# Optimization experiments

Hardware: AMD Instinct MI355X
Metric: run time of the kernel (lower is better)

## Reference

```python
import jax, jax.numpy as jnp
import numpy as np

L, B, D, H, P = 4096, 4, 1024, 16, 256
HD = D // H
EPS = 1e-5


def _layer_norm(x, g, b):
    m = jnp.mean(x, axis=-1, keepdims=True)
    v = jnp.mean(jnp.square(x - m), axis=-1, keepdims=True)
    return (x - m) / jnp.sqrt(v + EPS) * g + b


def setup_inputs() -> dict:
    key = jax.random.key(0)
    ks = jax.random.split(key, 8)
    w = lambda k, shape: jax.random.normal(k, shape, jnp.float32) * 0.02
    return {
        "query": jax.random.normal(ks[0], (L, B, D), jnp.float32),
        "q_w": w(ks[1], (D, D)), "q_b": jnp.zeros((D,), jnp.float32),
        "k_w": w(ks[2], (D, D)), "k_b": jnp.zeros((D,), jnp.float32),
        "v_w": w(ks[3], (D, D)), "v_b": jnp.zeros((D,), jnp.float32),
        "e_weight": w(ks[4], (1, H, P, HD)),
        "e_out_w": w(ks[5], (D, D)), "e_out_b": jnp.zeros((D,), jnp.float32),
        "ln_g": jnp.ones((D,), jnp.float32), "ln_b": jnp.zeros((D,), jnp.float32),
        "out_w": w(ks[6], (D, D)), "out_b": jnp.zeros((D,), jnp.float32),
    }


def reference(query, q_w, q_b, k_w, k_b, v_w, v_b, e_weight,
              e_out_w, e_out_b, ln_g, ln_b, out_w, out_b):
    scaling = HD ** -0.5
    # ---- _compute_kv (kv_same=True, no padding mask) ----
    # kv: (L,B,D) -> (B,H,HD,L)
    kvh = query.reshape(L, B, H, HD).transpose(1, 2, 3, 0)
    # pkv = relu(E @ (kv * scaling)) : (B,H,P,L)
    pkv = jax.nn.relu(jnp.einsum('hpd,bhdl->bhpl', e_weight[0], kvh * scaling))
    # kv = pkv @ kv^T : (B,H,P,HD)
    kv = jnp.einsum('bhpl,bhdl->bhpd', pkv, kvh)
    # -> (P,B,D), e_out linear, residual add of e_weight, layer norm
    kv = kv.transpose(2, 0, 1, 3).reshape(P, B, D)
    kv = kv @ e_out_w.T + e_out_b
    kv = kv.reshape(P, B, H, HD) + e_weight.transpose(2, 0, 1, 3)  # broadcast (P,1,H,HD)
    kv = _layer_norm(kv.reshape(P, B, D), ln_g, ln_b)  # (P,B,D)

    # ---- standard MHA against the compressed kv ----
    q = (query @ q_w.T + q_b) * scaling            # (L,B,D)
    k = kv @ k_w.T + k_b                           # (P,B,D)
    v = kv @ v_w.T + v_b                           # (P,B,D)
    qh = q.reshape(L, B, H, HD)
    kh = k.reshape(P, B, H, HD)
    vh = v.reshape(P, B, H, HD)
    logits = jnp.einsum('lbhd,pbhd->bhlp', qh, kh)
    probs = jax.nn.softmax(logits, axis=-1)
    attn = jnp.einsum('bhlp,pbhd->lbhd', probs, vh).reshape(L, B, D)
    return attn @ out_w.T + out_b
```

## Files before the change

kernel.cpp:

```cpp
#include <hip/hip_runtime.h>
#include <hip/hip_bf16.h>
#include <cstdint>
#include <cstddef>

#define LL 4096
#define BB 4
#define DD 1024
#define HH 16
#define PP 256
#define HDD 64
#define LC 16
#define LCHUNK 256

constexpr float kScaling = 0.125f;
constexpr float kEps = 1e-5f;

typedef __attribute__((ext_vector_type(8))) short bf16x8;
typedef __attribute__((ext_vector_type(4))) short short4v;
typedef __attribute__((ext_vector_type(4))) float f32x4;

#define MFMA16(a, b, c) __builtin_amdgcn_mfma_f32_16x16x32_bf16((a), (b), (c), 0, 0, 0)

__device__ __forceinline__ unsigned short f2bf(float f) {
  unsigned int u = __builtin_bit_cast(unsigned int, f);
  u += 0x7FFFu + ((u >> 16) & 1u);
  return (unsigned short)(u >> 16);
}

__device__ __forceinline__ void gll16(const void* g, void* l) {
  __builtin_amdgcn_global_load_lds(
      (const __attribute__((address_space(1))) unsigned int*)g,
      (__attribute__((address_space(3))) unsigned int*)l, 16, 0, 0);
}

__global__ __launch_bounds__(256) void k_cvt(const float* __restrict__ src,
                                             unsigned short* __restrict__ dst,
                                             int n8) {
  int i = blockIdx.x * 256 + threadIdx.x;
  if (i >= n8) return;
  const float4* s = (const float4*)(src + (size_t)i * 8);
  float4 a = s[0], b = s[1];
  bf16x8 o;
  o[0] = f2bf(a.x); o[1] = f2bf(a.y); o[2] = f2bf(a.z); o[3] = f2bf(a.w);
  o[4] = f2bf(b.x); o[5] = f2bf(b.y); o[6] = f2bf(b.z); o[7] = f2bf(b.w);
  *(bf16x8*)(dst + (size_t)i * 8) = o;
}

__global__ __launch_bounds__(256) void k_compress_mfma(
    const unsigned short* __restrict__ qbf, const unsigned short* __restrict__ ewbf,
    float* __restrict__ parts) {
  const int bh = blockIdx.x, lc = blockIdx.y;
  const int b = bh >> 4, h = bh & 15;
  const int tid = threadIdx.x, wv = tid >> 6, lane = tid & 63;
  const int fr = lane & 15, fg = lane >> 4;

  __shared__ __align__(16) char Xl[8192];
  __shared__ __align__(16) char Xtl[8192];
  __shared__ __align__(16) char Pl[32768];

  bf16x8 ef[4][2];
#pragma unroll
  for (int pt = 0; pt < 4; ++pt)
#pragma unroll
    for (int kc = 0; kc < 2; ++kc)
      ef[pt][kc] = *(const bf16x8*)(ewbf +
          (size_t)((h * PP + wv * 64 + pt * 16 + fr) * HDD) + kc * 32 + fg * 8);

  f32x4 acc[4][4];
#pragma unroll
  for (int i = 0; i < 4; ++i)
#pragma unroll
    for (int j = 0; j < 4; ++j) acc[i][j] = (f32x4){0.f, 0.f, 0.f, 0.f};

  const int l0 = lc * LCHUNK;
  for (int t = 0; t < 4; ++t) {
    __syncthreads();
#pragma unroll
    for (int j = 0; j < 2; ++j) {
      int u = tid + j * 256;
      int l = u >> 3, c8 = u & 7;
      bf16x8 val = *(const bf16x8*)(qbf +
          ((size_t)(l0 + t * 64 + l) * BB + b) * DD + h * HDD + c8 * 8);
      *(bf16x8*)(Xl + l * 128 + ((c8 ^ (l & 7)) << 4)) = val;
#pragma unroll
      for (int i = 0; i < 8; ++i) {
        int dd = c8 * 8 + i;
        *(short*)(Xtl + dd * 128 + ((((l >> 3) ^ (dd & 7) ^ (dd >> 3)) & 7) << 4) +
                  ((l & 7) << 1)) = val[i];
      }
    }
    __syncthreads();
#pragma unroll
    for (int lt = 0; lt < 4; ++lt) {
      int rl = lt * 16 + fr;
      bf16x8 xa0 = *(const bf16x8*)(Xl + rl * 128 + (((0 + fg) ^ (rl & 7)) << 4));
      bf16x8 xa1 = *(const bf16x8*)(Xl + rl * 128 + (((4 + fg) ^ (rl & 7)) << 4));
#pragma unroll
      for (int pt = 0; pt < 4; ++pt) {
        f32x4 s = (f32x4){0.f, 0.f, 0.f, 0.f};
        s = MFMA16(xa0, ef[pt][0], s);
        s = MFMA16(xa1, ef[pt][1], s);
        short4v pk;
#pragma unroll
        for (int r = 0; r < 4; ++r)
          pk[r] = (short)f2bf(fmaxf(s[r] * kScaling, 0.f));
        int p = wv * 64 + pt * 16 + fr;
        int lbase = lt * 16 + fg * 4;
        int slot = lbase >> 3;
        *(short4v*)(Pl + p * 128 + ((slot ^ (p & 7)) << 4) + ((lbase & 7) << 1)) = pk;
      }
    }
    asm volatile("s_waitcnt lgkmcnt(0)" ::: "memory");
    __builtin_amdgcn_sched_barrier(0);
#pragma unroll
    for (int kc = 0; kc < 2; ++kc) {
      bf16x8 pa[4], xb[4];
#pragma unroll
      for (int pt = 0; pt < 4; ++pt) {
        int p = wv * 64 + pt * 16 + fr;
        pa[pt] = *(const bf16x8*)(Pl + p * 128 + (((kc * 4 + fg) ^ (p & 7)) << 4));
      }
#pragma unroll
      for (int dt = 0; dt < 4; ++dt) {
        int dd = dt * 16 + fr;
        xb[dt] = *(const bf16x8*)(Xtl + dd * 128 +
                  ((((kc * 4 + fg) ^ (dd & 7) ^ (dd >> 3)) & 7) << 4));
      }
#pragma unroll
      for (int pt = 0; pt < 4; ++pt)
#pragma unroll
        for (int dt = 0; dt < 4; ++dt)
          acc[pt][dt] = MFMA16(pa[pt], xb[dt], acc[pt][dt]);
    }
  }
  float* op = parts + (size_t)(lc * 64 + bh) * PP * HDD;
#pragma unroll
  for (int pt = 0; pt < 4; ++pt)
#pragma unroll
    for (int dt = 0; dt < 4; ++dt)
#pragma unroll
      for (int r = 0; r < 4; ++r) {
        int p = wv * 64 + pt * 16 + fg * 4 + r;
        int dd = dt * 16 + fr;
        op[(size_t)p * HDD + dd] = acc[pt][dt][r];
      }
}

__global__ __launch_bounds__(256) void k_reduce(const float* __restrict__ parts,
                                                unsigned short* __restrict__ kv_raw_bf) {
  int i = blockIdx.x * 256 + threadIdx.x;
  float s = 0.f;
#pragma unroll
  for (int lcc = 0; lcc < LC; ++lcc) s += parts[(size_t)lcc * (64 * PP * HDD) + i];
  int d = i & 63, p = (i >> 6) & 255, bh = i >> 14;
  int b = bh >> 4, h = bh & 15;
  kv_raw_bf[(size_t)(p * BB + b) * DD + h * HDD + d] = f2bf(s);
}

template <int MODE, typename OUTT>
__device__ __forceinline__ void gemm_body(
    const unsigned short* __restrict__ A, const unsigned short* __restrict__ W,
    const float* __restrict__ bias, const float* __restrict__ ew,
    OUTT* __restrict__ C, int m0, int n0, char* Al, char* Bl) {
  const int tid = threadIdx.x;
  const int wv = tid >> 6, lane = tid & 63;
  const int fr = lane & 15, fg = lane >> 4;
  const int wr = wv >> 1, wc = wv & 1;

  f32x4 acc[4][4];
#pragma unroll
  for (int i = 0; i < 4; ++i)
#pragma unroll
    for (int j = 0; j < 4; ++j) acc[i][j] = (f32x4){0.f, 0.f, 0.f, 0.f};

  for (int k0 = 0; k0 < DD; k0 += 64) {
    __syncthreads();
#pragma unroll
    for (int j = 0; j < 4; ++j) {
      int u = tid + j * 256;
      int row = u >> 3, slot = u & 7;
      size_t gcol = (size_t)(k0 + 8 * (slot ^ (row & 7)));
      gll16(A + (size_t)(m0 + row) * DD + gcol, Al + u * 16);
      gll16(W + (size_t)(n0 + row) * DD + gcol, Bl + u * 16);
    }
    __syncthreads();
#pragma unroll
    for (int kc = 0; kc < 2; ++kc) {
      bf16x8 af[4], bfr[4];
#pragma unroll
      for (int mt = 0; mt < 4; ++mt) {
        int r = wr * 64 + mt * 16 + fr;
        af[mt] = *(const bf16x8*)(Al + r * 128 + (((kc * 4 + fg) ^ (r & 7)) << 4));
      }
#pragma unroll
      for (int nt = 0; nt < 4; ++nt) {
        int r = wc * 64 + nt * 16 + fr;
        bfr[nt] = *(const bf16x8*)(Bl + r * 128 + (((kc * 4 + fg) ^ (r & 7)) << 4));
      }
#pragma unroll
      for (int mt = 0; mt < 4; ++mt)
#pragma unroll
        for (int nt = 0; nt < 4; ++nt)
          acc[mt][nt] = MFMA16(af[mt], bfr[nt], acc[mt][nt]);
    }
  }

  float bs[4];
#pragma unroll
  for (int nt = 0; nt < 4; ++nt) bs[nt] = bias[n0 + wc * 64 + nt * 16 + fr];
#pragma unroll
  for (int mt = 0; mt < 4; ++mt)
#pragma unroll
    for (int nt = 0; nt < 4; ++nt) {
      int n = n0 + wc * 64 + nt * 16 + fr;
#pragma unroll
      for (int r = 0; r < 4; ++r) {
        int m = m0 + wr * 64 + mt * 16 + fg * 4 + r;
        float v = acc[mt][nt][r] + bs[nt];
        if (MODE == 1) v *= kScaling;
        if (MODE == 2) {
          int p = m >> 2, hh = n >> 6, d2 = n & 63;
          v += ew[(size_t)((hh << 8) + p) * HDD + d2];
        }
        if constexpr (sizeof(OUTT) == 2)
          C[(size_t)m * DD + n] = (OUTT)f2bf(v);
        else
          C[(size_t)m * DD + n] = v;
      }
    }
}

template <int MODE, typename OUTT>
__global__ __launch_bounds__(256) void k_gemm_mfma(
    const unsigned short* __restrict__ A, const unsigned short* __restrict__ W,
    const float* __restrict__ bias, const float* __restrict__ ew,
    OUTT* __restrict__ C) {
  __shared__ __align__(16) char Al[16384];
  __shared__ __align__(16) char Bl[16384];
  gemm_body<MODE, OUTT>(A, W, bias, ew, C, blockIdx.x * 128, blockIdx.y * 128, Al, Bl);
}

__global__ __launch_bounds__(256) void k_gemm_kv(
    const unsigned short* __restrict__ A,
    const unsigned short* __restrict__ Wk, const unsigned short* __restrict__ Wv,
    const float* __restrict__ kb, const float* __restrict__ vb,
    unsigned short* __restrict__ Ck, unsigned short* __restrict__ Cv) {
  __shared__ __align__(16) char Al[16384];
  __shared__ __align__(16) char Bl[16384];
  if (blockIdx.z == 0)
    gemm_body<0, unsigned short>(A, Wk, kb, nullptr, Ck,
                                 blockIdx.x * 128, blockIdx.y * 128, Al, Bl);
  else
    gemm_body<0, unsigned short>(A, Wv, vb, nullptr, Cv,
                                 blockIdx.x * 128, blockIdx.y * 128, Al, Bl);
}

__global__ __launch_bounds__(256) void k_ln(const float* __restrict__ x,
                                            const float* __restrict__ g,
                                            const float* __restrict__ bb,
                                            unsigned short* __restrict__ y) {
  const int r = blockIdx.x;
  const int tid = threadIdx.x;
  const float* xr = x + (size_t)r * DD;
  float4 v = *(const float4*)(xr + tid * 4);
  float s1 = v.x + v.y + v.z + v.w;
  float s2 = v.x * v.x + v.y * v.y + v.z * v.z + v.w * v.w;
#pragma unroll
  for (int off = 32; off > 0; off >>= 1) {
    s1 += __shfl_down(s1, off);
    s2 += __shfl_down(s2, off);
  }
  __shared__ float w1[4], w2[4];
  if ((tid & 63) == 0) { w1[tid >> 6] = s1; w2[tid >> 6] = s2; }
  __syncthreads();
  float S1 = w1[0] + w1[1] + w1[2] + w1[3];
  float S2 = w2[0] + w2[1] + w2[2] + w2[3];
  float mean = S1 * (1.f / DD);
  float var = S2 * (1.f / DD) - mean * mean;
  float rstd = rsqrtf(var + kEps);
  float4 gv = *(const float4*)(g + tid * 4);
  float4 bv = *(const float4*)(bb + tid * 4);
  short4v o;
  o[0] = (short)f2bf((v.x - mean) * rstd * gv.x + bv.x);
  o[1] = (short)f2bf((v.y - mean) * rstd * gv.y + bv.y);
  o[2] = (short)f2bf((v.z - mean) * rstd * gv.z + bv.z);
  o[3] = (short)f2bf((v.w - mean) * rstd * gv.w + bv.w);
  *(short4v*)(y + (size_t)r * DD + tid * 4) = o;
}

__global__ __launch_bounds__(512, 2) void k_attn_mfma(
    const unsigned short* __restrict__ qbf, const unsigned short* __restrict__ kbf,
    const unsigned short* __restrict__ vbf, unsigned short* __restrict__ attn) {
  const int bh = blockIdx.y;
  const int b = bh >> 4, h = bh & 15;
  const int tid = threadIdx.x, wv = tid >> 6, lane = tid & 63;
  const int fr = lane & 15, fg = lane >> 4;
  const int bl0 = blockIdx.x * 128;

  __shared__ __align__(16) char Kl[16384];
  __shared__ __align__(16) char Vt[16384];
  __shared__ __align__(16) char Pl[32768];

  const size_t qrow = ((size_t)(bl0 + wv * 16 + fr) * BB + b) * DD + h * HDD;
  bf16x8 qf0 = *(const bf16x8*)(qbf + qrow + fg * 8);
  bf16x8 qf1 = *(const bf16x8*)(qbf + qrow + 32 + fg * 8);

  f32x4 o[4];
#pragma unroll
  for (int dt = 0; dt < 4; ++dt) o[dt] = (f32x4){0.f, 0.f, 0.f, 0.f};
  float psum = 0.f;
  char* Pw = Pl + wv * 4096;

  for (int ph = 0; ph < 2; ++ph) {
    __syncthreads();
#pragma unroll
    for (int j = 0; j < 2; ++j) {
      int u = tid + j * 512;
      int p = u >> 3, slot = u & 7;
      gll16(kbf + ((size_t)((ph * 128 + p) * BB + b)) * DD + h * HDD +
                8 * (slot ^ (p & 7)),
            Kl + u * 16);
    }
#pragma unroll
    for (int j = 0; j < 2; ++j) {
      int u = tid + j * 512;
      int p = u >> 3, c8 = u & 7;
      bf16x8 val = *(const bf16x8*)(vbf +
          ((size_t)((ph * 128 + p) * BB + b)) * DD + h * HDD + c8 * 8);
      int pc = p >> 6, pl = p & 63;
#pragma unroll
      for (int i = 0; i < 8; ++i) {
        int dd = c8 * 8 + i;
        *(short*)(Vt + pc * 8192 + dd * 128 +
                  ((((pl >> 3) ^ (dd & 7) ^ (dd >> 3)) & 7) << 4) +
                  ((pl & 7) << 1)) = val[i];
      }
    }
    __syncthreads();

    f32x4 s[8];
    __builtin_amdgcn_s_setprio(1);
#pragma unroll
    for (int pt = 0; pt < 8; ++pt) {
      int pr = pt * 16 + fr;
      bf16x8 a0 = *(const bf16x8*)(Kl + pr * 128 + ((fg ^ (pr & 7)) << 4));
      bf16x8 a1 = *(const bf16x8*)(Kl + pr * 128 + (((4 + fg) ^ (pr & 7)) << 4));
      f32x4 acc = (f32x4){0.f, 0.f, 0.f, 0.f};
      acc = MFMA16(a0, qf0, acc);
      acc = MFMA16(a1, qf1, acc);
      s[pt] = acc;
    }
    __builtin_amdgcn_s_setprio(0);

#pragma unroll
    for (int pt = 0; pt < 8; ++pt) {
      float e0 = __expf(s[pt][0]), e1 = __expf(s[pt][1]);
      float e2 = __expf(s[pt][2]), e3 = __expf(s[pt][3]);
      psum += (e0 + e1) + (e2 + e3);
      short4v pk;
      pk[0] = (short)f2bf(e0); pk[1] = (short)f2bf(e1);
      pk[2] = (short)f2bf(e2); pk[3] = (short)f2bf(e3);
      int pbyte = (pt * 16 + fg * 4) * 2;
      int slot = pbyte >> 4, rem = pbyte & 15;
      *(short4v*)(Pw + fr * 256 + ((slot ^ (fr & 7)) << 4) + rem) = pk;
    }
    asm volatile("s_waitcnt lgkmcnt(0)" ::: "memory");
    __builtin_amdgcn_sched_barrier(0);

    __builtin_amdgcn_s_setprio(1);
#pragma unroll
    for (int kc = 0; kc < 4; ++kc) {
      int slot = kc * 4 + fg;
      bf16x8 pa = *(const bf16x8*)(Pw + fr * 256 + ((slot ^ (fr & 7)) << 4));
      int sl2 = (kc & 1) * 4 + fg;
#pragma unroll
      for (int dt = 0; dt < 4; ++dt) {
        int dd = dt * 16 + fr;
        bf16x8 vb = *(const bf16x8*)(Vt + (kc >> 1) * 8192 + dd * 128 +
                     (((sl2 ^ (dd & 7) ^ (dd >> 3)) & 7) << 4));
        o[dt] = MFMA16(pa, vb, o[dt]);
      }
    }
    __builtin_amdgcn_s_setprio(0);
  }

  psum += __shfl_xor(psum, 16);
  psum += __shfl_xor(psum, 32);

#pragma unroll
  for (int r = 0; r < 4; ++r) {
    int lloc = fg * 4 + r;
    float inv = 1.f / __shfl(psum, lloc);
    unsigned short* op = attn +
        ((size_t)(bl0 + wv * 16 + lloc) * BB + b) * DD + h * HDD;
#pragma unroll
    for (int dt = 0; dt < 4; ++dt)
      op[dt * 16 + fr] = f2bf(o[dt][r] * inv);
  }
}

extern "C" void kernel_launch(void* const* d_in, const int* in_sizes, int n_in,
                              void* d_out, int out_size, void* d_ws, size_t ws_size,
                              hipStream_t stream) {
  const float* query   = (const float*)d_in[0];
  const float* q_w     = (const float*)d_in[1];
  const float* q_b     = (const float*)d_in[2];
  const float* k_w     = (const float*)d_in[3];
  const float* k_b     = (const float*)d_in[4];
  const float* v_w     = (const float*)d_in[5];
  const float* v_b     = (const float*)d_in[6];
  const float* e_weight= (const float*)d_in[7];
  const float* e_out_w = (const float*)d_in[8];
  const float* e_out_b = (const float*)d_in[9];
  const float* ln_g    = (const float*)d_in[10];
  const float* ln_b    = (const float*)d_in[11];
  const float* out_w   = (const float*)d_in[12];
  const float* out_b   = (const float*)d_in[13];
  float* out = (float*)d_out;

  char* w = (char*)d_ws;
  float* parts            = (float*)w;
  unsigned short* q_bf    = (unsigned short*)w;
  unsigned short* attn_bf = (unsigned short*)(w + (32u << 20));
  unsigned short* query_bf= (unsigned short*)(w + (64u << 20));
  unsigned short* kv_raw  = (unsigned short*)(w + (96u << 20));
  float* kv_eo            = (float*)(w + (98u << 20));
  unsigned short* kv_ln   = (unsigned short*)(w + (102u << 20));
  unsigned short* k_buf   = (unsigned short*)(w + (104u << 20));
  unsigned short* v_buf   = (unsigned short*)(w + (106u << 20));
  unsigned short* wq  = (unsigned short*)(w + (108u << 20));
  unsigned short* wk  = (unsigned short*)(w + (110u << 20));
  unsigned short* wv_ = (unsigned short*)(w + (112u << 20));
  unsigned short* weo = (unsigned short*)(w + (114u << 20));
  unsigned short* wo  = (unsigned short*)(w + (116u << 20));
  unsigned short* ewb = (unsigned short*)(w + (118u << 20));

  k_cvt<<<8192, 256, 0, stream>>>(query, query_bf, 2097152);
  k_cvt<<<512, 256, 0, stream>>>(q_w, wq, 131072);
  k_cvt<<<512, 256, 0, stream>>>(k_w, wk, 131072);
  k_cvt<<<512, 256, 0, stream>>>(v_w, wv_, 131072);
  k_cvt<<<512, 256, 0, stream>>>(e_out_w, weo, 131072);
  k_cvt<<<512, 256, 0, stream>>>(out_w, wo, 131072);
  k_cvt<<<128, 256, 0, stream>>>(e_weight, ewb, 32768);

  k_compress_mfma<<<dim3(64, LC), 256, 0, stream>>>(query_bf, ewb, parts);
  k_reduce<<<4096, 256, 0, stream>>>(parts, kv_raw);
  k_gemm_mfma<2, float><<<dim3(8, 8), 256, 0, stream>>>(kv_raw, weo, e_out_b, e_weight, kv_eo);
  k_ln<<<PP * BB, 256, 0, stream>>>(kv_eo, ln_g, ln_b, kv_ln);
  k_gemm_mfma<1, unsigned short><<<dim3(128, 8), 256, 0, stream>>>(query_bf, wq, q_b, nullptr, q_bf);
  k_gemm_kv<<<dim3(8, 8, 2), 256, 0, stream>>>(kv_ln, wk, wv_, k_b, v_b, k_buf, v_buf);
  k_attn_mfma<<<dim3(32, 64), 512, 0, stream>>>(q_bf, k_buf, v_buf, attn_bf);
  k_gemm_mfma<0, float><<<dim3(128, 8), 256, 0, stream>>>(attn_bf, wo, out_b, nullptr, out);
}
```

Before: 247.9 us.

## Use 256x256 tiled GEMM with triple-buffered async loads for Q and output projections

Adds a 512-thread GEMM kernel that computes a 256x256 output tile per block. It uses a 128 KB LDS double/triple-staged pipeline with direct global-to-LDS loads, XOR-swizzled layout, and interleaved MFMA phases with barriers and priority hints. The large Q projection and output projection GEMMs now use it instead of the 128x128 kernel. This aims to raise arithmetic intensity and overlap memory with compute. In exchange, the 256-block grid may underfill the CUs, the LDS footprint is large, and the register pressure is high.

```diff
diff --git a/kernel.cpp b/kernel.cpp
--- a/kernel.cpp
+++ b/kernel.cpp
@@ -253,6 +253,152 @@
   else
     gemm_body<0, unsigned short>(A, Wv, vb, nullptr, Cv,
                                  blockIdx.x * 128, blockIdx.y * 128, Al, Bl);
+}
+
+template <int MODE, typename OUTT>
+__global__ __launch_bounds__(512, 2) void k_gemm256(
+    const unsigned short* __restrict__ A, const unsigned short* __restrict__ W,
+    const float* __restrict__ bias, OUTT* __restrict__ C) {
+  __shared__ __align__(16) char lds[131072];
+  const int tid = threadIdx.x;
+  const int wv = tid >> 6, lane = tid & 63;
+  const int fr = lane & 15, fg = lane >> 4;
+  const int wm = wv >> 2, wn = wv & 3;
+  const int m0 = blockIdx.x * 256, n0 = blockIdx.y * 256;
+  const int srow = tid >> 2, sslot = tid & 3;
+
+  auto stageHalf = [&](const unsigned short* __restrict__ G, int g0, int colbase,
+                       int dstBase) {
+#pragma unroll
+    for (int j = 0; j < 2; ++j) {
+      int row = srow + j * 128;
+      int gs = sslot ^ ((row >> 1) & 3);
+      gll16(G + (size_t)(g0 + row) * DD + colbase + gs * 8,
+            lds + dstBase + (tid + j * 512) * 16);
+    }
+  };
+  auto rdA = [&](int mf, int kc, int cb) -> bf16x8 {
+    int r = wm * 128 + mf * 16 + fr;
+    return *(const bf16x8*)(lds + cb + kc * 16384 + r * 64 +
+                            ((fg ^ ((r >> 1) & 3)) << 4));
+  };
+  auto rdB = [&](int nf, int kc, int cb) -> bf16x8 {
+    int r = wn * 64 + nf * 16 + fr;
+    return *(const bf16x8*)(lds + cb + 32768 + kc * 16384 + r * 64 +
+                            ((fg ^ ((r >> 1) & 3)) << 4));
+  };
+
+  f32x4 acc[8][4];
+#pragma unroll
+  for (int i = 0; i < 8; ++i)
+#pragma unroll
+    for (int j = 0; j < 4; ++j) acc[i][j] = (f32x4){0.f, 0.f, 0.f, 0.f};
+  bf16x8 a[4], b[4];
+
+  stageHalf(A, m0, 0, 0);
+  stageHalf(W, n0, 0, 32768);
+  stageHalf(A, m0, 32, 16384);
+  stageHalf(W, n0, 32, 32768 + 16384);
+  stageHalf(A, m0, 64, 65536);
+  stageHalf(W, n0, 64, 65536 + 32768);
+  asm volatile("s_waitcnt vmcnt(4)" ::: "memory");
+  __builtin_amdgcn_s_barrier();
+
+  const int NT = DD / 64;
+  for (int t = 0; t < NT; ++t) {
+    const int cb = (t & 1) << 16;
+    const int nb = cb ^ 65536;
+    const int k1 = (t + 1) * 64, k2 = (t + 2) * 64;
+
+#pragma unroll
+    for (int i = 0; i < 4; ++i) a[i] = rdA(i, 0, cb);
+#pragma unroll
+    for (int i = 0; i < 4; ++i) b[i] = rdB(i, 0, cb);
+    if (t + 1 < NT) stageHalf(A, m0, k1 + 32, nb + 16384);
+    __builtin_amdgcn_s_barrier();
+    asm volatile("s_waitcnt lgkmcnt(0)" ::: "memory");
+    __builtin_amdgcn_sched_barrier(0);
+    __builtin_amdgcn_s_setprio(1);
+#pragma unroll
+    for (int mf = 0; mf < 4; ++mf)
+#pragma unroll
+      for (int nf = 0; nf < 4; ++nf)
+        acc[mf][nf] = MFMA16(a[mf], b[nf], acc[mf][nf]);
+    __builtin_amdgcn_s_setprio(0);
+    __builtin_amdgcn_s_barrier();
+
+#pragma unroll
+    for (int i = 0; i < 4; ++i) a[i] = rdA(4 + i, 0, cb);
+    if (t + 1 < NT) stageHalf(W, n0, k1 + 32, nb + 32768 + 16384);
+    __builtin_amdgcn_s_barrier();
+    asm volatile("s_waitcnt lgkmcnt(0)" ::: "memory");
+    __builtin_amdgcn_sched_barrier(0);
+    __builtin_amdgcn_s_setprio(1);
+#pragma unroll
+    for (int mf = 0; mf < 4; ++mf)
+#pragma unroll
+      for (int nf = 0; nf < 4; ++nf)
+        acc[4 + mf][nf] = MFMA16(a[mf], b[nf], acc[4 + mf][nf]);
+    __builtin_amdgcn_s_setprio(0);
+    __builtin_amdgcn_s_barrier();
+
+#pragma unroll
+    for (int i = 0; i < 4; ++i) a[i] = rdA(i, 1, cb);
+#pragma unroll
+    for (int i = 0; i < 4; ++i) b[i] = rdB(i, 1, cb);
+    if (t + 2 < NT) stageHalf(A, m0, k2, cb);
+    __builtin_amdgcn_s_barrier();
+    asm volatile("s_waitcnt lgkmcnt(0)" ::: "memory");
+    __builtin_amdgcn_sched_barrier(0);
+    __builtin_amdgcn_s_setprio(1);
+#pragma unroll
+    for (int mf = 0; mf < 4; ++mf)
+#pragma unroll
+      for (int nf = 0; nf < 4; ++nf)
+        acc[mf][nf] = MFMA16(a[mf], b[nf], acc[mf][nf]);
+    __builtin_amdgcn_s_setprio(0);
+    __builtin_amdgcn_s_barrier();
+
+#pragma unroll
+    for (int i = 0; i < 4; ++i) a[i] = rdA(4 + i, 1, cb);
+    if (t + 2 < NT) stageHalf(W, n0, k2, cb + 32768);
+    __builtin_amdgcn_s_barrier();
+    asm volatile("s_waitcnt lgkmcnt(0)" ::: "memory");
+    __builtin_amdgcn_sched_barrier(0);
+    __builtin_amdgcn_s_setprio(1);
+#pragma unroll
+    for (int mf = 0; mf < 4; ++mf)
+#pragma unroll
+      for (int nf = 0; nf < 4; ++nf)
+        acc[4 + mf][nf] = MFMA16(a[mf], b[nf], acc[4 + mf][nf]);
+    __builtin_amdgcn_s_setprio(0);
+    if (t + 2 < NT) {
+      asm volatile("s_waitcnt vmcnt(4)" ::: "memory");
+    } else if (t + 1 < NT) {
+      asm volatile("s_waitcnt vmcnt(0)" ::: "memory");
+    }
+    __builtin_amdgcn_s_barrier();
+  }
+
+  float bs[4];
+#pragma unroll
+  for (int nf = 0; nf < 4; ++nf) bs[nf] = bias[n0 + wn * 64 + nf * 16 + fr];
+#pragma unroll
+  for (int mf = 0; mf < 8; ++mf)
+#pragma unroll
+    for (int nf = 0; nf < 4; ++nf) {
+      int n = n0 + wn * 64 + nf * 16 + fr;
+#pragma unroll
+      for (int r = 0; r < 4; ++r) {
+        int m = m0 + wm * 128 + mf * 16 + fg * 4 + r;
+        float v = acc[mf][nf][r] + bs[nf];
+        if (MODE == 1) v *= kScaling;
+        if constexpr (sizeof(OUTT) == 2)
+          C[(size_t)m * DD + n] = (OUTT)f2bf(v);
+        else
+          C[(size_t)m * DD + n] = v;
+      }
+    }
 }
 
 __global__ __launch_bounds__(256) void k_ln(const float* __restrict__ x,
@@ -447,8 +593,8 @@
   k_reduce<<<4096, 256, 0, stream>>>(parts, kv_raw);
   k_gemm_mfma<2, float><<<dim3(8, 8), 256, 0, stream>>>(kv_raw, weo, e_out_b, e_weight, kv_eo);
   k_ln<<<PP * BB, 256, 0, stream>>>(kv_eo, ln_g, ln_b, kv_ln);
-  k_gemm_mfma<1, unsigned short><<<dim3(128, 8), 256, 0, stream>>>(query_bf, wq, q_b, nullptr, q_bf);
+  k_gemm256<1, unsigned short><<<dim3(64, 4), 512, 0, stream>>>(query_bf, wq, q_b, q_bf);
   k_gemm_kv<<<dim3(8, 8, 2), 256, 0, stream>>>(kv_ln, wk, wv_, k_b, v_b, k_buf, v_buf);
   k_attn_mfma<<<dim3(32, 64), 512, 0, stream>>>(q_bf, k_buf, v_buf, attn_bf);
-  k_gemm_mfma<0, float><<<dim3(128, 8), 256, 0, stream>>>(attn_bf, wo, out_b, nullptr, out);
-}
+  k_gemm256<0, float><<<dim3(64, 4), 512, 0, stream>>>(attn_bf, wo, out_b, out);
+}
```

New measurement: 238.1 us. 4.0% less time.
